# Kernel optimization log

Hardware: AMD Instinct MI355X
Metric: run time of the kernel (lower is better)

## Reference

```python
import jax, jax.numpy as jnp
import numpy as np

B, D, H, C = 32768, 512, 512, 128  # batch, input_dim, hidden, n_classes (nurse==doctor)
L = 3  # 3 PAN layers and 3 shared FC layers
BN_EPS = 1e-5


def setup_inputs() -> dict:
    key = jax.random.key(0)
    ks = iter(jax.random.split(key, 64))

    def rn(shape, scale):
        return (jax.random.normal(next(ks), shape, jnp.float32) * scale)

    inv = lambda fan: 1.0 / np.sqrt(fan)

    x = jax.random.normal(next(ks), (B, D), jnp.float32)
    s_n = jax.random.randint(next(ks), (B,), 0, C)
    s_d = jax.random.randint(next(ks), (B,), 0, C)
    # cols -4 / -3 carry integer staffing caps (s_nurse_max, s_doctor_max)
    x = x.at[:, -4].set(s_n.astype(jnp.float32)).at[:, -3].set(s_d.astype(jnp.float32))

    inp = {
        'x': x,
        # ClinicalPAN params, stacked over L=3 layers (and 3 branches)
        'pbw': rn((L, 3, D, 32), inv(D)), 'pbb': jnp.zeros((L, 3, 32), jnp.float32),
        'paw1': rn((L, D, 64), inv(D)),  'pab1': jnp.zeros((L, 64), jnp.float32),
        'paw2': rn((L, 64, 32), inv(64)),'pab2': jnp.zeros((L, 32), jnp.float32),
        'piw1': rn((L, D, 16), inv(D)),  'pib1': jnp.zeros((L, 16), jnp.float32),
        'piw2': rn((L, 16, 1), inv(16)), 'pib2': jnp.zeros((L, 1), jnp.float32),
        'pfw': rn((L, 96, D), inv(96)),  'pfb': jnp.zeros((L, D), jnp.float32),
        'pgw': rn((L, D, D), inv(D)),    'pgb': jnp.zeros((L, D), jnp.float32),
        # shared Linear + BatchNorm1d (eval mode: running stats), stacked
        'fcw': rn((L, D, H), inv(D)),    'fcb': jnp.zeros((L, H), jnp.float32),
        'bng': jnp.ones((L, H), jnp.float32),  'bnb': jnp.zeros((L, H), jnp.float32),
        'bnm': jnp.zeros((L, H), jnp.float32), 'bnv': jnp.ones((L, H), jnp.float32),
        # heads
        'nhw1': rn((H, 64), inv(H)), 'nhb1': jnp.zeros((64,), jnp.float32),
        'nhw2': rn((64, C), inv(64)), 'nhb2': jnp.zeros((C,), jnp.float32),
        'dhw1': rn((H, 64), inv(H)), 'dhb1': jnp.zeros((64,), jnp.float32),
        'dhw2': rn((64, C), inv(64)), 'dhb2': jnp.zeros((C,), jnp.float32),
        'wtw1': rn((H, 64), inv(H)), 'wtb1': jnp.zeros((64,), jnp.float32),
        'wtw2': rn((64, 1), inv(64)), 'wtb2': jnp.zeros((1,), jnp.float32),
    }
    return inp


def reference(x, pbw, pbb, paw1, pab1, paw2, pab2, piw1, pib1, piw2, pib2,
              pfw, pfb, pgw, pgb, fcw, fcb, bng, bnb, bnm, bnv,
              nhw1, nhb1, nhw2, nhb2, dhw1, dhb1, dhw2, dhb2,
              wtw1, wtb1, wtw2, wtb2):
    # integer caps (constants w.r.t. grad)
    s_n = jax.lax.stop_gradient(x[:, -4]).astype(jnp.int32)
    s_d = jax.lax.stop_gradient(x[:, -3]).astype(jnp.int32)

    h = x
    for l in range(L):  # ClinicalPAN stack (dropout = identity in eval)
        cw = jax.nn.sigmoid(jax.nn.relu(h @ paw1[l] + pab1[l]) @ paw2[l] + pab2[l])   # [B,32]
        ci = jax.nn.sigmoid(jax.nn.relu(h @ piw1[l] + pib1[l]) @ piw2[l] + pib2[l])   # [B,1]
        feats = jax.nn.relu(jnp.einsum('bd,kdh->bkh', h, pbw[l]) + pbb[l][None])      # [B,3,32]
        weighted = feats * (cw * ci)[:, None, :]                                       # [B,3,32]
        fused = weighted.reshape(h.shape[0], 96) @ pfw[l] + pfb[l]                     # [B,D]
        gate = jax.nn.sigmoid(h @ pgw[l] + pgb[l])
        h = fused + gate * h

    for i in range(L):  # shared Linear -> BN(eval) -> ReLU
        z = h @ fcw[i] + fcb[i]
        z = bng[i] * (z - bnm[i]) * jax.lax.rsqrt(bnv[i] + BN_EPS) + bnb[i]
        h = jax.nn.relu(z)

    nurse_logits = jax.nn.relu(h @ nhw1 + nhb1) @ nhw2 + nhb2   # [B,C]
    doctor_logits = jax.nn.relu(h @ dhw1 + dhb1) @ dhw2 + dhb2  # [B,C]
    wait_time = jax.nn.relu(h @ wtw1 + wtb1) @ wtw2 + wtb2      # [B,1]

    idx = jnp.arange(C)
    nm = (idx[None, :] <= s_n[:, None]).astype(nurse_logits.dtype)
    dm = (idx[None, :] <= s_d[:, None]).astype(doctor_logits.dtype)
    NEG = jnp.asarray(-1e9, nurse_logits.dtype)
    nurse_logits = nurse_logits * nm + (1.0 - nm) * NEG
    doctor_logits = doctor_logits * dm + (1.0 - dm) * NEG
    return nurse_logits, doctor_logits, wait_time
```

## Files before the change

### kernel.cpp

```cpp
#include <hip/hip_runtime.h>

#define DI __device__ __forceinline__

typedef short bf16x8 __attribute__((ext_vector_type(8)));
typedef float f32x4  __attribute__((ext_vector_type(4)));

#define MFMA(a,b,c) __builtin_amdgcn_mfma_f32_16x16x32_bf16(a,b,c,0,0,0)

constexpr int    SZ_WT = 512*80;
constexpr int    SZ_WB = 512*96;
constexpr int    SZ_WF = 96*512;
constexpr int    SZ_WG = 512*512;
constexpr int    SZ_WC = 512*512;
constexpr size_t OFF_WT  = 0;
constexpr size_t OFF_WB  = OFF_WT + 3*(size_t)SZ_WT;
constexpr size_t OFF_WF  = OFF_WB + 3*(size_t)SZ_WB;
constexpr size_t OFF_WG  = OFF_WF + 3*(size_t)SZ_WF;
constexpr size_t OFF_WC  = OFF_WG + 3*(size_t)SZ_WG;
constexpr size_t OFF_WH  = OFF_WC + 3*(size_t)SZ_WC;
constexpr size_t OFF_WH2 = OFF_WH + (size_t)512*192;
constexpr size_t WS_TOTAL= OFF_WH2 + (size_t)128*256;

DI short f2b(float f){ unsigned u; __builtin_memcpy(&u,&f,4); u += 0x7fffu + ((u>>16)&1u); return (short)(u>>16); }
DI float b2f(short s){ unsigned u = ((unsigned)(unsigned short)s)<<16; float f; __builtin_memcpy(&f,&u,4); return f; }
DI float sigm(float x){ return 1.f/(1.f+__expf(-x)); }
DI unsigned pk2(float a, float b){
  return (unsigned)(unsigned short)f2b(a) | ((unsigned)(unsigned short)f2b(b) << 16);
}

__global__ __launch_bounds__(256) void prep_weights(
    const float* __restrict__ pbw,  const float* __restrict__ paw1,
    const float* __restrict__ piw1, const float* __restrict__ pfw,
    const float* __restrict__ pgw,  const float* __restrict__ fcw,
    const float* __restrict__ nhw1, const float* __restrict__ nhw2,
    const float* __restrict__ dhw1, const float* __restrict__ dhw2,
    const float* __restrict__ wtw1, short* __restrict__ ws)
{
  size_t t = (size_t)blockIdx.x*256 + threadIdx.x;
  if (t >= WS_TOTAL) return;
  float v = 0.f;
  if (t < OFF_WB) {
    int q=(int)t; int ly=q/SZ_WT; int qq=q%SZ_WT;
    int j=qq&7, lane=(qq>>3)&63, tile=qq>>9, kt=tile&15, nt=tile>>4;
    int k=kt*32+((lane>>4)<<3)+j, n=nt*16+(lane&15);
    v = (n<64) ? paw1[((size_t)ly*512+k)*64+n] : piw1[((size_t)ly*512+k)*16+(n-64)];
  } else if (t < OFF_WF) {
    int q=(int)(t-OFF_WB); int ly=q/SZ_WB; int qq=q%SZ_WB;
    int j=qq&7, lane=(qq>>3)&63, tile=qq>>9, kt=tile&15, nt=tile>>4;
    int k=kt*32+((lane>>4)<<3)+j, c=nt*16+(lane&15);
    v = pbw[(((size_t)ly*3+(c>>5))*512+k)*32+(c&31)];
  } else if (t < OFF_WG) {
    int q=(int)(t-OFF_WF); int ly=q/SZ_WF; int qq=q%SZ_WF;
    int j=qq&7, lane=(qq>>3)&63, tile=qq>>9, kt=tile%3, nt=tile/3;
    int k=kt*32+((lane>>4)<<3)+j, n=nt*16+(lane&15);
    v = pfw[((size_t)ly*96+k)*512+n];
  } else if (t < OFF_WC) {
    int q=(int)(t-OFF_WG); int ly=q/SZ_WG; int qq=q%SZ_WG;
    int j=qq&7, lane=(qq>>3)&63, tile=qq>>9, kt=tile&15, nt=tile>>4;
    int k=kt*32+((lane>>4)<<3)+j, n=nt*16+(lane&15);
    v = pgw[((size_t)ly*512+k)*512+n];
  } else if (t < OFF_WH) {
    int q=(int)(t-OFF_WC); int ly=q/SZ_WC; int qq=q%SZ_WC;
    int j=qq&7, lane=(qq>>3)&63, tile=qq>>9, kt=tile&15, nt=tile>>4;
    int k=kt*32+((lane>>4)<<3)+j, n=nt*16+(lane&15);
    v = fcw[((size_t)ly*512+k)*512+n];
  } else if (t < OFF_WH2) {
    int qq=(int)(t-OFF_WH);
    int j=qq&7, lane=(qq>>3)&63, tile=qq>>9, kt=tile&15, nt=tile>>4;
    int k=kt*32+((lane>>4)<<3)+j, n=nt*16+(lane&15);
    v = (n<64) ? nhw1[(size_t)k*64+n] : (n<128) ? dhw1[(size_t)k*64+(n-64)] : wtw1[(size_t)k*64+(n-128)];
  } else {
    int qq=(int)(t-OFF_WH2);
    int j=qq&7, lane=(qq>>3)&63, tile=qq>>9, kt=tile&3, nt=tile>>2;
    int k=kt*32+((lane>>4)<<3)+j, n=nt*16+(lane&15);
    if (k<64) v = (n<128) ? nhw2[(size_t)k*128+n] : 0.f;
    else      v = (n>=128)? dhw2[(size_t)(k-64)*128+(n-128)] : 0.f;
  }
  ws[t] = f2b(v);
}

__global__ __launch_bounds__(1024, 4) void pan_main(
  const float* __restrict__ x,
  const float* __restrict__ pbb,  const float* __restrict__ pab1,
  const float* __restrict__ paw2, const float* __restrict__ pab2,
  const float* __restrict__ pib1, const float* __restrict__ piw2,
  const float* __restrict__ pib2, const float* __restrict__ pfb,
  const float* __restrict__ pgb,  const float* __restrict__ fcb,
  const float* __restrict__ bng,  const float* __restrict__ bnb,
  const float* __restrict__ bnm,  const float* __restrict__ bnv,
  const float* __restrict__ nhb1, const float* __restrict__ nhb2,
  const float* __restrict__ dhb1, const float* __restrict__ dhb2,
  const float* __restrict__ wtb1, const float* __restrict__ wtw2,
  const float* __restrict__ wtb2,
  const short* __restrict__ ws, float* __restrict__ out)
{
  __shared__ __align__(16) char lds[163840];
  char* sH = lds;
  char* sU = lds + 131072;

  const int tid  = threadIdx.x;
  const int wave = tid >> 6;
  const int l    = tid & 63;
  const int lr   = l & 15;
  const int lb   = l >> 4;
  const int swzA = (lr & 7) << 4;
  const size_t row0 = (size_t)blockIdx.x * 128;

  #pragma unroll 2
  for (int c = tid; c < 8192; c += 1024) {
    int row = c >> 6, k0 = (c & 63) << 3;
    const float4* s0 = (const float4*)(x + (row0 + row)*512 + k0);
    float4 f0 = s0[0], f1 = s0[1];
    bf16x8 p;
    p[0]=f2b(f0.x); p[1]=f2b(f0.y); p[2]=f2b(f0.z); p[3]=f2b(f0.w);
    p[4]=f2b(f1.x); p[5]=f2b(f1.y); p[6]=f2b(f1.z); p[7]=f2b(f1.w);
    *(bf16x8*)(sH + row*1024 + ((k0*2) ^ ((row&7)<<4))) = p;
  }
  __syncthreads();

  auto ldA = [&](int rt, int kt) -> bf16x8 {
    int row = rt*16 + lr;
    return *(const bf16x8*)(sH + row*1024 + ((kt*64 + lb*16) ^ swzA));
  };
  auto ldB = [&](const short* W, int K32, int nt, int kt) -> bf16x8 {
    return *(const bf16x8*)(W + (((size_t)(nt*K32 + kt))*64 + l)*8);
  };
  auto ldH = [&](int row, int col) -> float {
    return b2f(*(const short*)(sH + row*1024 + ((col*2) ^ ((row&7)<<4))));
  };
  const f32x4 FZ = {0.f,0.f,0.f,0.f};

  for (int ly = 0; ly < 3; ++ly) {
    if (wave < 10) {
      const short* W = ws + OFF_WT + (size_t)ly*SZ_WT;
      const int nt = wave % 5, rh = wave / 5;
      f32x4 acc[4];
      #pragma unroll
      for (int rt=0;rt<4;++rt) acc[rt] = FZ;
      #pragma unroll 2
      for (int kt=0;kt<16;++kt) {
        bf16x8 b = ldB(W,16,nt,kt);
        #pragma unroll
        for (int rt=0;rt<4;++rt) acc[rt] = MFMA(ldA(rh*4+rt,kt), b, acc[rt]);
      }
      const int col = nt*16 + lr;
      const float bias = (col<64) ? pab1[ly*64+col] : pib1[ly*16+(col-64)];
      #pragma unroll
      for (int rt=0;rt<4;++rt)
        #pragma unroll
        for (int jj=0;jj<4;++jj) {
          int row = rh*64 + rt*16 + lb*4 + jj;
          *(short*)(sU + row*160 + col*2) = f2b(fmaxf(acc[rt][jj]+bias, 0.f));
        }
    }
    __syncthreads();
    if (tid < 128) {
      float s = pib2[ly];
      bf16x8 t0 = *(const bf16x8*)(sU + tid*160 + 128);
      bf16x8 t1 = *(const bf16x8*)(sU + tid*160 + 144);
      #pragma unroll
      for (int i=0;i<8;++i) {
        s += b2f(t0[i]) * piw2[ly*16+i];
        s += b2f(t1[i]) * piw2[ly*16+8+i];
      }
      *(float*)(sU + 20480 + tid*4) = sigm(s);
    }
    __syncthreads();
    {
      const int r = tid>>3, j0 = (tid&7)<<2;
      float a4[4];
      #pragma unroll
      for (int i=0;i<4;++i) a4[i] = pab2[ly*32 + j0 + i];
      #pragma unroll 2
      for (int k8=0;k8<8;++k8) {
        bf16x8 tv8 = *(const bf16x8*)(sU + r*160 + k8*16);
        #pragma unroll
        for (int i8=0;i8<8;++i8) {
          float tv = b2f(tv8[i8]);
          float4 wr = *(const float4*)(paw2 + ((size_t)ly*64 + k8*8+i8)*32 + j0);
          a4[0]=fmaf(tv,wr.x,a4[0]); a4[1]=fmaf(tv,wr.y,a4[1]);
          a4[2]=fmaf(tv,wr.z,a4[2]); a4[3]=fmaf(tv,wr.w,a4[3]);
        }
      }
      const float civ = *(const float*)(sU + 20480 + r*4);
      #pragma unroll
      for (int i=0;i<4;++i)
        *(short*)(sU + 20992 + (r*32 + j0 + i)*2) = f2b(sigm(a4[i]) * civ);
    }
    __syncthreads();
    unsigned wpk[4][2];
    if (wave < 12) {
      const short* W = ws + OFF_WB + (size_t)ly*SZ_WB;
      const int nt = wave % 6, rh = wave / 6;
      f32x4 acc[4];
      #pragma unroll
      for (int rt=0;rt<4;++rt) acc[rt] = FZ;
      #pragma unroll 2
      for (int kt=0;kt<16;++kt) {
        bf16x8 b = ldB(W,16,nt,kt);
        #pragma unroll
        for (int rt=0;rt<4;++rt) acc[rt] = MFMA(ldA(rh*4+rt,kt), b, acc[rt]);
      }
      const int col = nt*16 + lr;
      const float bias = pbb[ly*96 + col];
      #pragma unroll
      for (int rt=0;rt<4;++rt) {
        float w4[4];
        #pragma unroll
        for (int jj=0;jj<4;++jj) {
          int row = rh*64 + rt*16 + lb*4 + jj;
          float cc = b2f(*(const short*)(sU + 20992 + (row*32 + (col&31))*2));
          w4[jj] = fmaxf(acc[rt][jj]+bias, 0.f) * cc;
        }
        wpk[rt][0] = pk2(w4[0], w4[1]);
        wpk[rt][1] = pk2(w4[2], w4[3]);
      }
    }
    __syncthreads();
    if (wave < 12) {
      const int nt = wave % 6, rh = wave / 6;
      const int col = nt*16 + lr;
      #pragma unroll
      for (int rt=0;rt<4;++rt)
        #pragma unroll
        for (int p=0;p<2;++p) {
          int r0 = rh*64 + rt*16 + lb*4 + p*2;
          unsigned v = wpk[rt][p];
          *(short*)(sU + r0*256     + ((col*2) ^ ((r0    &7)<<4))) = (short)(v & 0xffff);
          *(short*)(sU + (r0+1)*256 + ((col*2) ^ (((r0+1)&7)<<4))) = (short)(v >> 16);
        }
    }
    __syncthreads();
    unsigned pk[2][8][2];
    {
      const short* Wg = ws + OFF_WG + (size_t)ly*SZ_WG;
      const short* Wf = ws + OFF_WF + (size_t)ly*SZ_WF;
      #pragma unroll
      for (int p=0; p<2; ++p) {
        const int c = wave*2 + p;
        f32x4 acc[8];
        #pragma unroll
        for (int rt=0;rt<8;++rt) acc[rt] = FZ;
        #pragma unroll 2
        for (int kt=0;kt<16;++kt) {
          bf16x8 b = ldB(Wg,16, c, kt);
          #pragma unroll
          for (int rt=0;rt<8;++rt) acc[rt] = MFMA(ldA(rt,kt), b, acc[rt]);
        }
        const int col = c*16 + lr;
        const float gb = pgb[ly*512+col];
        const float fb = pfb[ly*512+col];
        #pragma unroll
        for (int rt=0;rt<8;++rt)
          #pragma unroll
          for (int jj=0;jj<4;++jj) {
            int row = rt*16 + lb*4 + jj;
            acc[rt][jj] = sigm(acc[rt][jj]+gb)*ldH(row,col) + fb;
          }
        #pragma unroll 1
        for (int kt=0;kt<3;++kt) {
          bf16x8 b = ldB(Wf,3, c, kt);
          #pragma unroll
          for (int rt=0;rt<8;++rt) {
            int row = rt*16 + lr;
            bf16x8 a = *(const bf16x8*)(sU + row*256 + ((kt*64 + lb*16) ^ swzA));
            acc[rt] = MFMA(a,b,acc[rt]);
          }
        }
        #pragma unroll
        for (int rt=0;rt<8;++rt) {
          pk[p][rt][0] = pk2(acc[rt][0], acc[rt][1]);
          pk[p][rt][1] = pk2(acc[rt][2], acc[rt][3]);
        }
      }
    }
    __syncthreads();
    #pragma unroll
    for (int p=0;p<2;++p) {
      const int col = (wave*2+p)*16 + lr;
      #pragma unroll
      for (int rt=0;rt<8;++rt)
        #pragma unroll
        for (int q=0;q<2;++q) {
          int r0 = rt*16 + lb*4 + q*2;
          unsigned v = pk[p][rt][q];
          *(short*)(sH + r0*1024     + ((col*2) ^ ((r0    &7)<<4))) = (short)(v & 0xffff);
          *(short*)(sH + (r0+1)*1024 + ((col*2) ^ (((r0+1)&7)<<4))) = (short)(v >> 16);
        }
    }
    __syncthreads();
  }

  for (int fi=0; fi<3; ++fi) {
    const short* W = ws + OFF_WC + (size_t)fi*SZ_WC;
    unsigned pk[2][8][2];
    #pragma unroll
    for (int p=0; p<2; ++p) {
      const int c = wave*2 + p;
      f32x4 acc[8];
      #pragma unroll
      for (int rt=0;rt<8;++rt) acc[rt] = FZ;
      #pragma unroll 2
      for (int kt=0;kt<16;++kt) {
        bf16x8 b = ldB(W,16, c, kt);
        #pragma unroll
        for (int rt=0;rt<8;++rt) acc[rt] = MFMA(ldA(rt,kt), b, acc[rt]);
      }
      const int col = c*16 + lr;
      const float sc = bng[fi*512+col] * rsqrtf(bnv[fi*512+col] + 1e-5f);
      const float of = bnb[fi*512+col] - bnm[fi*512+col]*sc;
      const float bb = fcb[fi*512+col];
      #pragma unroll
      for (int rt=0;rt<8;++rt) {
        float z0 = fmaxf((acc[rt][0] + bb)*sc + of, 0.f);
        float z1 = fmaxf((acc[rt][1] + bb)*sc + of, 0.f);
        float z2 = fmaxf((acc[rt][2] + bb)*sc + of, 0.f);
        float z3 = fmaxf((acc[rt][3] + bb)*sc + of, 0.f);
        pk[p][rt][0] = pk2(z0, z1);
        pk[p][rt][1] = pk2(z2, z3);
      }
    }
    __syncthreads();
    #pragma unroll
    for (int p=0;p<2;++p) {
      const int col = (wave*2+p)*16 + lr;
      #pragma unroll
      for (int rt=0;rt<8;++rt)
        #pragma unroll
        for (int q=0;q<2;++q) {
          int r0 = rt*16 + lb*4 + q*2;
          unsigned v = pk[p][rt][q];
          *(short*)(sH + r0*1024     + ((col*2) ^ ((r0    &7)<<4))) = (short)(v & 0xffff);
          *(short*)(sH + (r0+1)*1024 + ((col*2) ^ (((r0+1)&7)<<4))) = (short)(v >> 16);
        }
    }
    __syncthreads();
  }

  unsigned hk[8][2];
  if (wave < 12) {
    const short* W = ws + OFF_WH;
    f32x4 acc[8];
    #pragma unroll
    for (int rt=0;rt<8;++rt) acc[rt] = FZ;
    #pragma unroll 2
    for (int kt=0;kt<16;++kt) {
      bf16x8 b = ldB(W,16,wave,kt);
      #pragma unroll
      for (int rt=0;rt<8;++rt) acc[rt] = MFMA(ldA(rt,kt), b, acc[rt]);
    }
    const int col = wave*16 + lr;
    const float bias = (col<64) ? nhb1[col] : (col<128) ? dhb1[col-64] : wtb1[col-128];
    #pragma unroll
    for (int rt=0;rt<8;++rt) {
      hk[rt][0] = pk2(fmaxf(acc[rt][0]+bias,0.f), fmaxf(acc[rt][1]+bias,0.f));
      hk[rt][1] = pk2(fmaxf(acc[rt][2]+bias,0.f), fmaxf(acc[rt][3]+bias,0.f));
    }
  }
  __syncthreads();
  if (wave < 12) {
    const int col = wave*16 + lr;
    #pragma unroll
    for (int rt=0;rt<8;++rt)
      #pragma unroll
      for (int q=0;q<2;++q) {
        int r0 = rt*16 + lb*4 + q*2;
        unsigned v = hk[rt][q];
        *(short*)(lds + r0*384     + ((col*2) ^ ((r0    &7)<<4))) = (short)(v & 0xffff);
        *(short*)(lds + (r0+1)*384 + ((col*2) ^ (((r0+1)&7)<<4))) = (short)(v >> 16);
      }
  }
  __syncthreads();
  {
    const short* W2 = ws + OFF_WH2;
    f32x4 acc[8];
    #pragma unroll
    for (int rt=0;rt<8;++rt) acc[rt] = FZ;
    #pragma unroll 2
    for (int kt=0;kt<4;++kt) {
      bf16x8 b = ldB(W2,4, wave, kt);
      #pragma unroll
      for (int rt=0;rt<8;++rt) {
        int row = rt*16 + lr;
        bf16x8 a = *(const bf16x8*)(lds + row*384 + ((kt*64 + lb*16) ^ swzA));
        acc[rt] = MFMA(a,b,acc[rt]);
      }
    }
    const int col2 = wave*16 + lr;
    const bool isn = col2 < 128;
    const int cc = col2 & 127;
    const float bias = isn ? nhb2[cc] : dhb2[cc];
    const size_t obase = isn ? (size_t)0 : (size_t)4194304;
    #pragma unroll
    for (int rt=0;rt<8;++rt)
      #pragma unroll
      for (int jj=0;jj<4;++jj) {
        int row = rt*16 + lb*4 + jj;
        size_t rg = row0 + row;
        float2 caps = *(const float2*)(x + rg*512 + 508);
        int cap = (int)(isn ? caps.x : caps.y);
        float v = acc[rt][jj] + bias;
        out[obase + rg*128 + cc] = (cc <= cap) ? v : -1e9f;
      }
  }
  if (tid < 128) {
    float s = wtb2[0];
    #pragma unroll 2
    for (int k8=0;k8<8;++k8) {
      bf16x8 hv = *(const bf16x8*)(lds + tid*384 + ((256 + k8*16) ^ ((tid&7)<<4)));
      #pragma unroll
      for (int i=0;i<8;++i) s += b2f(hv[i]) * wtw2[k8*8+i];
    }
    out[(size_t)8388608 + row0 + tid] = s;
  }
}

extern "C" void kernel_launch(void* const* d_in, const int* in_sizes, int n_in,
                              void* d_out, int out_size, void* d_ws, size_t ws_size,
                              hipStream_t stream) {
  const float* x    = (const float*)d_in[0];
  const float* pbw  = (const float*)d_in[1];
  const float* pbb  = (const float*)d_in[2];
  const float* paw1 = (const float*)d_in[3];
  const float* pab1 = (const float*)d_in[4];
  const float* paw2 = (const float*)d_in[5];
  const float* pab2 = (const float*)d_in[6];
  const float* piw1 = (const float*)d_in[7];
  const float* pib1 = (const float*)d_in[8];
  const float* piw2 = (const float*)d_in[9];
  const float* pib2 = (const float*)d_in[10];
  const float* pfw  = (const float*)d_in[11];
  const float* pfb  = (const float*)d_in[12];
  const float* pgw  = (const float*)d_in[13];
  const float* pgb  = (const float*)d_in[14];
  const float* fcw  = (const float*)d_in[15];
  const float* fcb  = (const float*)d_in[16];
  const float* bng  = (const float*)d_in[17];
  const float* bnb  = (const float*)d_in[18];
  const float* bnm  = (const float*)d_in[19];
  const float* bnv  = (const float*)d_in[20];
  const float* nhw1 = (const float*)d_in[21];
  const float* nhb1 = (const float*)d_in[22];
  const float* nhw2 = (const float*)d_in[23];
  const float* nhb2 = (const float*)d_in[24];
  const float* dhw1 = (const float*)d_in[25];
  const float* dhb1 = (const float*)d_in[26];
  const float* dhw2 = (const float*)d_in[27];
  const float* dhb2 = (const float*)d_in[28];
  const float* wtw1 = (const float*)d_in[29];
  const float* wtb1 = (const float*)d_in[30];
  const float* wtw2 = (const float*)d_in[31];
  const float* wtb2 = (const float*)d_in[32];
  short* ws  = (short*)d_ws;
  float* out = (float*)d_out;

  prep_weights<<<(int)((WS_TOTAL + 255)/256), 256, 0, stream>>>(
      pbw, paw1, piw1, pfw, pgw, fcw, nhw1, nhw2, dhw1, dhw2, wtw1, ws);
  pan_main<<<256, 1024, 0, stream>>>(
      x, pbb, pab1, paw2, pab2, pib1, piw2, pib2, pfb, pgb, fcb,
      bng, bnb, bnm, bnv, nhb1, nhb2, dhb1, dhb2, wtb1, wtw2, wtb2, ws, out);
}
```

Baseline: 373.5 us.

## Halve block tile to 64 rows and 512 threads so two blocks fit per CU

```diff
diff --git a/kernel.cpp b/kernel.cpp
--- a/kernel.cpp
+++ b/kernel.cpp
@@ -79,7 +79,7 @@
   ws[t] = f2b(v);
 }
 
-__global__ __launch_bounds__(1024, 4) void pan_main(
+__global__ __launch_bounds__(512, 4) void pan_main(
   const float* __restrict__ x,
   const float* __restrict__ pbb,  const float* __restrict__ pab1,
   const float* __restrict__ paw2, const float* __restrict__ pab2,
@@ -94,9 +94,9 @@
   const float* __restrict__ wtb2,
   const short* __restrict__ ws, float* __restrict__ out)
 {
-  __shared__ __align__(16) char lds[163840];
+  __shared__ __align__(16) char lds[81920];
   char* sH = lds;
-  char* sU = lds + 131072;
+  char* sU = lds + 65536;
 
   const int tid  = threadIdx.x;
   const int wave = tid >> 6;
@@ -104,10 +104,10 @@
   const int lr   = l & 15;
   const int lb   = l >> 4;
   const int swzA = (lr & 7) << 4;
-  const size_t row0 = (size_t)blockIdx.x * 128;
+  const size_t row0 = (size_t)blockIdx.x * 64;
 
   #pragma unroll 2
-  for (int c = tid; c < 8192; c += 1024) {
+  for (int c = tid; c < 4096; c += 512) {
     int row = c >> 6, k0 = (c & 63) << 3;
     const float4* s0 = (const float4*)(x + (row0 + row)*512 + k0);
     float4 f0 = s0[0], f1 = s0[1];
@@ -131,30 +131,29 @@
   const f32x4 FZ = {0.f,0.f,0.f,0.f};
 
   for (int ly = 0; ly < 3; ++ly) {
-    if (wave < 10) {
+    if (wave < 5) {
       const short* W = ws + OFF_WT + (size_t)ly*SZ_WT;
-      const int nt = wave % 5, rh = wave / 5;
       f32x4 acc[4];
       #pragma unroll
       for (int rt=0;rt<4;++rt) acc[rt] = FZ;
       #pragma unroll 2
       for (int kt=0;kt<16;++kt) {
-        bf16x8 b = ldB(W,16,nt,kt);
-        #pragma unroll
-        for (int rt=0;rt<4;++rt) acc[rt] = MFMA(ldA(rh*4+rt,kt), b, acc[rt]);
-      }
-      const int col = nt*16 + lr;
+        bf16x8 b = ldB(W,16,wave,kt);
+        #pragma unroll
+        for (int rt=0;rt<4;++rt) acc[rt] = MFMA(ldA(rt,kt), b, acc[rt]);
+      }
+      const int col = wave*16 + lr;
       const float bias = (col<64) ? pab1[ly*64+col] : pib1[ly*16+(col-64)];
       #pragma unroll
       for (int rt=0;rt<4;++rt)
         #pragma unroll
         for (int jj=0;jj<4;++jj) {
-          int row = rh*64 + rt*16 + lb*4 + jj;
+          int row = rt*16 + lb*4 + jj;
           *(short*)(sU + row*160 + col*2) = f2b(fmaxf(acc[rt][jj]+bias, 0.f));
         }
     }
     __syncthreads();
-    if (tid < 128) {
+    if (tid < 64) {
       float s = pib2[ly];
       bf16x8 t0 = *(const bf16x8*)(sU + tid*160 + 128);
       bf16x8 t1 = *(const bf16x8*)(sU + tid*160 + 144);
@@ -163,7 +162,7 @@
         s += b2f(t0[i]) * piw2[ly*16+i];
         s += b2f(t1[i]) * piw2[ly*16+8+i];
       }
-      *(float*)(sU + 20480 + tid*4) = sigm(s);
+      *(float*)(sU + 10240 + tid*4) = sigm(s);
     }
     __syncthreads();
     {
@@ -182,34 +181,33 @@
           a4[2]=fmaf(tv,wr.z,a4[2]); a4[3]=fmaf(tv,wr.w,a4[3]);
         }
       }
-      const float civ = *(const float*)(sU + 20480 + r*4);
+      const float civ = *(const float*)(sU + 10240 + r*4);
       #pragma unroll
       for (int i=0;i<4;++i)
-        *(short*)(sU + 20992 + (r*32 + j0 + i)*2) = f2b(sigm(a4[i]) * civ);
+        *(short*)(sU + 10496 + (r*32 + j0 + i)*2) = f2b(sigm(a4[i]) * civ);
     }
     __syncthreads();
     unsigned wpk[4][2];
-    if (wave < 12) {
+    if (wave < 6) {
       const short* W = ws + OFF_WB + (size_t)ly*SZ_WB;
-      const int nt = wave % 6, rh = wave / 6;
       f32x4 acc[4];
       #pragma unroll
       for (int rt=0;rt<4;++rt) acc[rt] = FZ;
       #pragma unroll 2
       for (int kt=0;kt<16;++kt) {
-        bf16x8 b = ldB(W,16,nt,kt);
-        #pragma unroll
-        for (int rt=0;rt<4;++rt) acc[rt] = MFMA(ldA(rh*4+rt,kt), b, acc[rt]);
-      }
-      const int col = nt*16 + lr;
+        bf16x8 b = ldB(W,16,wave,kt);
+        #pragma unroll
+        for (int rt=0;rt<4;++rt) acc[rt] = MFMA(ldA(rt,kt), b, acc[rt]);
+      }
+      const int col = wave*16 + lr;
       const float bias = pbb[ly*96 + col];
       #pragma unroll
       for (int rt=0;rt<4;++rt) {
         float w4[4];
         #pragma unroll
         for (int jj=0;jj<4;++jj) {
-          int row = rh*64 + rt*16 + lb*4 + jj;
-          float cc = b2f(*(const short*)(sU + 20992 + (row*32 + (col&31))*2));
+          int row = rt*16 + lb*4 + jj;
+          float cc = b2f(*(const short*)(sU + 10496 + (row*32 + (col&31))*2));
           w4[jj] = fmaxf(acc[rt][jj]+bias, 0.f) * cc;
         }
         wpk[rt][0] = pk2(w4[0], w4[1]);
@@ -217,73 +215,83 @@
       }
     }
     __syncthreads();
-    if (wave < 12) {
-      const int nt = wave % 6, rh = wave / 6;
-      const int col = nt*16 + lr;
+    if (wave < 6) {
+      const int col = wave*16 + lr;
       #pragma unroll
       for (int rt=0;rt<4;++rt)
         #pragma unroll
         for (int p=0;p<2;++p) {
-          int r0 = rh*64 + rt*16 + lb*4 + p*2;
+          int r0 = rt*16 + lb*4 + p*2;
           unsigned v = wpk[rt][p];
           *(short*)(sU + r0*256     + ((col*2) ^ ((r0    &7)<<4))) = (short)(v & 0xffff);
           *(short*)(sU + (r0+1)*256 + ((col*2) ^ (((r0+1)&7)<<4))) = (short)(v >> 16);
         }
     }
     __syncthreads();
-    unsigned pk[2][8][2];
+    unsigned pk[4][4][2];
     {
       const short* Wg = ws + OFF_WG + (size_t)ly*SZ_WG;
       const short* Wf = ws + OFF_WF + (size_t)ly*SZ_WF;
       #pragma unroll
       for (int p=0; p<2; ++p) {
-        const int c = wave*2 + p;
-        f32x4 acc[8];
-        #pragma unroll
-        for (int rt=0;rt<8;++rt) acc[rt] = FZ;
+        f32x4 acc[4][2];
+        #pragma unroll
+        for (int rt=0;rt<4;++rt) { acc[rt][0]=FZ; acc[rt][1]=FZ; }
         #pragma unroll 2
         for (int kt=0;kt<16;++kt) {
-          bf16x8 b = ldB(Wg,16, c, kt);
+          bf16x8 b0 = ldB(Wg,16, wave*4+p*2+0, kt);
+          bf16x8 b1 = ldB(Wg,16, wave*4+p*2+1, kt);
           #pragma unroll
-          for (int rt=0;rt<8;++rt) acc[rt] = MFMA(ldA(rt,kt), b, acc[rt]);
-        }
-        const int col = c*16 + lr;
-        const float gb = pgb[ly*512+col];
-        const float fb = pfb[ly*512+col];
-        #pragma unroll
-        for (int rt=0;rt<8;++rt)
+          for (int rt=0;rt<4;++rt) {
+            bf16x8 a = ldA(rt,kt);
+            acc[rt][0] = MFMA(a,b0,acc[rt][0]);
+            acc[rt][1] = MFMA(a,b1,acc[rt][1]);
+          }
+        }
+        #pragma unroll
+        for (int c2=0;c2<2;++c2) {
+          const int col = (wave*4+p*2+c2)*16 + lr;
+          const float gb = pgb[ly*512+col];
+          const float fb = pfb[ly*512+col];
           #pragma unroll
-          for (int jj=0;jj<4;++jj) {
-            int row = rt*16 + lb*4 + jj;
-            acc[rt][jj] = sigm(acc[rt][jj]+gb)*ldH(row,col) + fb;
-          }
+          for (int rt=0;rt<4;++rt)
+            #pragma unroll
+            for (int jj=0;jj<4;++jj) {
+              int row = rt*16 + lb*4 + jj;
+              acc[rt][c2][jj] = sigm(acc[rt][c2][jj]+gb)*ldH(row,col) + fb;
+            }
+        }
         #pragma unroll 1
         for (int kt=0;kt<3;++kt) {
-          bf16x8 b = ldB(Wf,3, c, kt);
+          bf16x8 b0 = ldB(Wf,3, wave*4+p*2+0, kt);
+          bf16x8 b1 = ldB(Wf,3, wave*4+p*2+1, kt);
           #pragma unroll
-          for (int rt=0;rt<8;++rt) {
+          for (int rt=0;rt<4;++rt) {
             int row = rt*16 + lr;
             bf16x8 a = *(const bf16x8*)(sU + row*256 + ((kt*64 + lb*16) ^ swzA));
-            acc[rt] = MFMA(a,b,acc[rt]);
+            acc[rt][0] = MFMA(a,b0,acc[rt][0]);
+            acc[rt][1] = MFMA(a,b1,acc[rt][1]);
           }
         }
         #pragma unroll
-        for (int rt=0;rt<8;++rt) {
-          pk[p][rt][0] = pk2(acc[rt][0], acc[rt][1]);
-          pk[p][rt][1] = pk2(acc[rt][2], acc[rt][3]);
-        }
+        for (int c2=0;c2<2;++c2)
+          #pragma unroll
+          for (int rt=0;rt<4;++rt) {
+            pk[p*2+c2][rt][0] = pk2(acc[rt][c2][0], acc[rt][c2][1]);
+            pk[p*2+c2][rt][1] = pk2(acc[rt][c2][2], acc[rt][c2][3]);
+          }
       }
     }
     __syncthreads();
     #pragma unroll
-    for (int p=0;p<2;++p) {
-      const int col = (wave*2+p)*16 + lr;
-      #pragma unroll
-      for (int rt=0;rt<8;++rt)
+    for (int ci2=0;ci2<4;++ci2) {
+      const int col = (wave*4+ci2)*16 + lr;
+      #pragma unroll
+      for (int rt=0;rt<4;++rt)
         #pragma unroll
         for (int q=0;q<2;++q) {
           int r0 = rt*16 + lb*4 + q*2;
-          unsigned v = pk[p][rt][q];
+          unsigned v = pk[ci2][rt][q];
           *(short*)(sH + r0*1024     + ((col*2) ^ ((r0    &7)<<4))) = (short)(v & 0xffff);
           *(short*)(sH + (r0+1)*1024 + ((col*2) ^ (((r0+1)&7)<<4))) = (short)(v >> 16);
         }
@@ -293,43 +301,50 @@
 
   for (int fi=0; fi<3; ++fi) {
     const short* W = ws + OFF_WC + (size_t)fi*SZ_WC;
-    unsigned pk[2][8][2];
+    unsigned pk[4][4][2];
     #pragma unroll
     for (int p=0; p<2; ++p) {
-      const int c = wave*2 + p;
-      f32x4 acc[8];
-      #pragma unroll
-      for (int rt=0;rt<8;++rt) acc[rt] = FZ;
+      f32x4 acc[4][2];
+      #pragma unroll
+      for (int rt=0;rt<4;++rt) { acc[rt][0]=FZ; acc[rt][1]=FZ; }
       #pragma unroll 2
       for (int kt=0;kt<16;++kt) {
-        bf16x8 b = ldB(W,16, c, kt);
-        #pragma unroll
-        for (int rt=0;rt<8;++rt) acc[rt] = MFMA(ldA(rt,kt), b, acc[rt]);
-      }
-      const int col = c*16 + lr;
-      const float sc = bng[fi*512+col] * rsqrtf(bnv[fi*512+col] + 1e-5f);
-      const float of = bnb[fi*512+col] - bnm[fi*512+col]*sc;
-      const float bb = fcb[fi*512+col];
-      #pragma unroll
-      for (int rt=0;rt<8;++rt) {
-        float z0 = fmaxf((acc[rt][0] + bb)*sc + of, 0.f);
-        float z1 = fmaxf((acc[rt][1] + bb)*sc + of, 0.f);
-        float z2 = fmaxf((acc[rt][2] + bb)*sc + of, 0.f);
-        float z3 = fmaxf((acc[rt][3] + bb)*sc + of, 0.f);
-        pk[p][rt][0] = pk2(z0, z1);
-        pk[p][rt][1] = pk2(z2, z3);
+        bf16x8 b0 = ldB(W,16, wave*4+p*2+0, kt);
+        bf16x8 b1 = ldB(W,16, wave*4+p*2+1, kt);
+        #pragma unroll
+        for (int rt=0;rt<4;++rt) {
+          bf16x8 a = ldA(rt,kt);
+          acc[rt][0] = MFMA(a,b0,acc[rt][0]);
+          acc[rt][1] = MFMA(a,b1,acc[rt][1]);
+        }
+      }
+      #pragma unroll
+      for (int c2=0;c2<2;++c2) {
+        const int col = (wave*4+p*2+c2)*16 + lr;
+        const float sc = bng[fi*512+col] * rsqrtf(bnv[fi*512+col] + 1e-5f);
+        const float of = bnb[fi*512+col] - bnm[fi*512+col]*sc;
+        const float bb = fcb[fi*512+col];
+        #pragma unroll
+        for (int rt=0;rt<4;++rt) {
+          float z0 = fmaxf((acc[rt][c2][0] + bb)*sc + of, 0.f);
+          float z1 = fmaxf((acc[rt][c2][1] + bb)*sc + of, 0.f);
+          float z2 = fmaxf((acc[rt][c2][2] + bb)*sc + of, 0.f);
+          float z3 = fmaxf((acc[rt][c2][3] + bb)*sc + of, 0.f);
+          pk[p*2+c2][rt][0] = pk2(z0, z1);
+          pk[p*2+c2][rt][1] = pk2(z2, z3);
+        }
       }
     }
     __syncthreads();
     #pragma unroll
-    for (int p=0;p<2;++p) {
-      const int col = (wave*2+p)*16 + lr;
-      #pragma unroll
-      for (int rt=0;rt<8;++rt)
+    for (int ci2=0;ci2<4;++ci2) {
+      const int col = (wave*4+ci2)*16 + lr;
+      #pragma unroll
+      for (int rt=0;rt<4;++rt)
         #pragma unroll
         for (int q=0;q<2;++q) {
           int r0 = rt*16 + lb*4 + q*2;
-          unsigned v = pk[p][rt][q];
+          unsigned v = pk[ci2][rt][q];
           *(short*)(sH + r0*1024     + ((col*2) ^ ((r0    &7)<<4))) = (short)(v & 0xffff);
           *(short*)(sH + (r0+1)*1024 + ((col*2) ^ (((r0+1)&7)<<4))) = (short)(v >> 16);
         }
@@ -337,73 +352,108 @@
     __syncthreads();
   }
 
-  unsigned hk[8][2];
-  if (wave < 12) {
+  unsigned hkA[4][2], hkB[4][2];
+  {
     const short* W = ws + OFF_WH;
-    f32x4 acc[8];
+    {
+      f32x4 acc[4];
+      #pragma unroll
+      for (int rt=0;rt<4;++rt) acc[rt] = FZ;
+      #pragma unroll 2
+      for (int kt=0;kt<16;++kt) {
+        bf16x8 b = ldB(W,16,wave,kt);
+        #pragma unroll
+        for (int rt=0;rt<4;++rt) acc[rt] = MFMA(ldA(rt,kt), b, acc[rt]);
+      }
+      const int col = wave*16 + lr;
+      const float bias = (col<64) ? nhb1[col] : dhb1[col-64];
+      #pragma unroll
+      for (int rt=0;rt<4;++rt) {
+        hkA[rt][0] = pk2(fmaxf(acc[rt][0]+bias,0.f), fmaxf(acc[rt][1]+bias,0.f));
+        hkA[rt][1] = pk2(fmaxf(acc[rt][2]+bias,0.f), fmaxf(acc[rt][3]+bias,0.f));
+      }
+    }
+    if (wave < 4) {
+      f32x4 acc[4];
+      #pragma unroll
+      for (int rt=0;rt<4;++rt) acc[rt] = FZ;
+      #pragma unroll 2
+      for (int kt=0;kt<16;++kt) {
+        bf16x8 b = ldB(W,16, 8+wave, kt);
+        #pragma unroll
+        for (int rt=0;rt<4;++rt) acc[rt] = MFMA(ldA(rt,kt), b, acc[rt]);
+      }
+      const int col = (8+wave)*16 + lr;
+      const float bias = wtb1[col-128];
+      #pragma unroll
+      for (int rt=0;rt<4;++rt) {
+        hkB[rt][0] = pk2(fmaxf(acc[rt][0]+bias,0.f), fmaxf(acc[rt][1]+bias,0.f));
+        hkB[rt][1] = pk2(fmaxf(acc[rt][2]+bias,0.f), fmaxf(acc[rt][3]+bias,0.f));
+      }
+    }
+  }
+  __syncthreads();
+  {
     #pragma unroll
-    for (int rt=0;rt<8;++rt) acc[rt] = FZ;
-    #pragma unroll 2
-    for (int kt=0;kt<16;++kt) {
-      bf16x8 b = ldB(W,16,wave,kt);
-      #pragma unroll
-      for (int rt=0;rt<8;++rt) acc[rt] = MFMA(ldA(rt,kt), b, acc[rt]);
-    }
-    const int col = wave*16 + lr;
-    const float bias = (col<64) ? nhb1[col] : (col<128) ? dhb1[col-64] : wtb1[col-128];
-    #pragma unroll
-    for (int rt=0;rt<8;++rt) {
-      hk[rt][0] = pk2(fmaxf(acc[rt][0]+bias,0.f), fmaxf(acc[rt][1]+bias,0.f));
-      hk[rt][1] = pk2(fmaxf(acc[rt][2]+bias,0.f), fmaxf(acc[rt][3]+bias,0.f));
-    }
-  }
-  __syncthreads();
-  if (wave < 12) {
-    const int col = wave*16 + lr;
-    #pragma unroll
-    for (int rt=0;rt<8;++rt)
+    for (int rt=0;rt<4;++rt)
       #pragma unroll
       for (int q=0;q<2;++q) {
         int r0 = rt*16 + lb*4 + q*2;
-        unsigned v = hk[rt][q];
-        *(short*)(lds + r0*384     + ((col*2) ^ ((r0    &7)<<4))) = (short)(v & 0xffff);
-        *(short*)(lds + (r0+1)*384 + ((col*2) ^ (((r0+1)&7)<<4))) = (short)(v >> 16);
-      }
+        int cA = wave*16 + lr;
+        unsigned v = hkA[rt][q];
+        *(short*)(lds + r0*384     + ((cA*2) ^ ((r0    &7)<<4))) = (short)(v & 0xffff);
+        *(short*)(lds + (r0+1)*384 + ((cA*2) ^ (((r0+1)&7)<<4))) = (short)(v >> 16);
+      }
+    if (wave < 4) {
+      #pragma unroll
+      for (int rt=0;rt<4;++rt)
+        #pragma unroll
+        for (int q=0;q<2;++q) {
+          int r0 = rt*16 + lb*4 + q*2;
+          int cB = (8+wave)*16 + lr;
+          unsigned v = hkB[rt][q];
+          *(short*)(lds + r0*384     + ((cB*2) ^ ((r0    &7)<<4))) = (short)(v & 0xffff);
+          *(short*)(lds + (r0+1)*384 + ((cB*2) ^ (((r0+1)&7)<<4))) = (short)(v >> 16);
+        }
+    }
   }
   __syncthreads();
   {
     const short* W2 = ws + OFF_WH2;
-    f32x4 acc[8];
     #pragma unroll
-    for (int rt=0;rt<8;++rt) acc[rt] = FZ;
-    #pragma unroll 2
-    for (int kt=0;kt<4;++kt) {
-      bf16x8 b = ldB(W2,4, wave, kt);
-      #pragma unroll
-      for (int rt=0;rt<8;++rt) {
-        int row = rt*16 + lr;
-        bf16x8 a = *(const bf16x8*)(lds + row*384 + ((kt*64 + lb*16) ^ swzA));
-        acc[rt] = MFMA(a,b,acc[rt]);
-      }
-    }
-    const int col2 = wave*16 + lr;
-    const bool isn = col2 < 128;
-    const int cc = col2 & 127;
-    const float bias = isn ? nhb2[cc] : dhb2[cc];
-    const size_t obase = isn ? (size_t)0 : (size_t)4194304;
-    #pragma unroll
-    for (int rt=0;rt<8;++rt)
-      #pragma unroll
-      for (int jj=0;jj<4;++jj) {
-        int row = rt*16 + lb*4 + jj;
-        size_t rg = row0 + row;
-        float2 caps = *(const float2*)(x + rg*512 + 508);
-        int cap = (int)(isn ? caps.x : caps.y);
-        float v = acc[rt][jj] + bias;
-        out[obase + rg*128 + cc] = (cc <= cap) ? v : -1e9f;
-      }
-  }
-  if (tid < 128) {
+    for (int p=0;p<2;++p) {
+      f32x4 acc[4];
+      #pragma unroll
+      for (int rt=0;rt<4;++rt) acc[rt] = FZ;
+      #pragma unroll 2
+      for (int kt=0;kt<4;++kt) {
+        bf16x8 b = ldB(W2,4, wave*2+p, kt);
+        #pragma unroll
+        for (int rt=0;rt<4;++rt) {
+          int row = rt*16 + lr;
+          bf16x8 a = *(const bf16x8*)(lds + row*384 + ((kt*64 + lb*16) ^ swzA));
+          acc[rt] = MFMA(a,b,acc[rt]);
+        }
+      }
+      const int col2 = (wave*2+p)*16 + lr;
+      const bool isn = col2 < 128;
+      const int cc = col2 & 127;
+      const float bias = isn ? nhb2[cc] : dhb2[cc];
+      const size_t obase = isn ? (size_t)0 : (size_t)4194304;
+      #pragma unroll
+      for (int rt=0;rt<4;++rt)
+        #pragma unroll
+        for (int jj=0;jj<4;++jj) {
+          int row = rt*16 + lb*4 + jj;
+          size_t rg = row0 + row;
+          float2 caps = *(const float2*)(x + rg*512 + 508);
+          int cap = (int)(isn ? caps.x : caps.y);
+          float v = acc[rt][jj] + bias;
+          out[obase + rg*128 + cc] = (cc <= cap) ? v : -1e9f;
+        }
+    }
+  }
+  if (tid < 64) {
     float s = wtb2[0];
     #pragma unroll 2
     for (int k8=0;k8<8;++k8) {
@@ -456,7 +506,7 @@
 
   prep_weights<<<(int)((WS_TOTAL + 255)/256), 256, 0, stream>>>(
       pbw, paw1, piw1, pfw, pgw, fcw, nhw1, nhw2, dhw1, dhw2, wtw1, ws);
-  pan_main<<<256, 1024, 0, stream>>>(
+  pan_main<<<512, 512, 0, stream>>>(
       x, pbb, pab1, paw2, pab2, pib1, piw2, pib2, pfb, pgb, fcb,
       bng, bnb, bnm, bnv, nhb1, nhb2, dhb1, dhb2, wtb1, wtw2, wtb2, ws, out);
 }
```

After: 330.1 us. 11.6% less time.
